# Kernel tuning notes

Measured on AMD Instinct MI355X. Metric: run time of the kernel, lower is better.

## Reference

```python
import jax, jax.numpy as jnp
import numpy as np

B, C, H, W = 8, 512, 32, 32
HEADS, TOPK = 8, 4


def setup_inputs() -> dict:
    key = jax.random.key(0)
    k1, k2 = jax.random.split(key, 2)
    x = jax.random.normal(k1, (B, C, H, W), dtype=jnp.float32)
    W_qkv = jax.random.normal(k2, (C, 3 * C), dtype=jnp.float32) / np.sqrt(C).astype(np.float32)
    b_qkv = jnp.zeros((3 * C,), dtype=jnp.float32)
    return {"x": x, "W_qkv": W_qkv, "b_qkv": b_qkv}


def reference(x, W_qkv, b_qkv):
    B_, C_, H_, W_ = x.shape
    h = HEADS
    d = C_ // h
    N = H_ * W_
    # (B, C, H, W) -> (B, N, C)
    xt = x.reshape(B_, C_, N).transpose(0, 2, 1)
    qkv = (xt @ W_qkv + b_qkv).reshape(B_, N, 3, h, d).transpose(2, 0, 3, 1, 4)
    q, k, v = qkv[0], qkv[1], qkv[2]            # each (B, h, N, d)
    attn = jnp.einsum('bhid,bhjd->bhij', q, k)  # dense (B, h, N, N) scores
    topk_w, topk_i = jax.lax.top_k(attn, TOPK)  # (B, h, N, K), sorted desc like torch.topk
    # gather v along token axis per (b, h): v_sel[b,h,i,t] = v[b,h,topk_i[b,h,i,t]]
    gather_bh = jax.vmap(jax.vmap(lambda vv, ii: vv[ii]))
    v_sel = gather_bh(v, topk_i)                # (B, h, N, K, d)
    w = jax.nn.softmax(topk_w, axis=-1)
    weighted_v = jnp.einsum('bhik,bhikd->bhid', w, v_sel)  # (B, h, N, d)
    out = (weighted_v * q).sum(axis=2)          # (B, h, d): original sums over tokens
    # original: out.transpose(1,2).reshape(B,C,H,W) -- only valid when H*W==1;
    # we return the same data flattened to (B, C).
    return out.transpose(0, 2, 1).reshape(B_, C_)
```

## Files before the change

### kernel.cpp

```cpp
#include <hip/hip_runtime.h>

#define NEG_INF (-3.402823466e+38f)

constexpr int Bc = 8, Cc = 512, Hc = 8, Dc = 64, Nc = 1024;
constexpr size_t QSZ = (size_t)Bc * Hc * Nc * Dc;
constexpr size_t XTSZ = (size_t)8192 * 512;
constexpr size_t WTSZ = (size_t)1536 * 512;

typedef __attribute__((ext_vector_type(8))) short short8;
typedef __attribute__((ext_vector_type(4))) float f32x4;
typedef unsigned short ushort_t;
typedef unsigned int uint_t;

__device__ __forceinline__ ushort_t f2bf(float x) {
  uint_t u = __float_as_uint(x);
  u += 0x7FFFu + ((u >> 16) & 1u);
  return (ushort_t)(u >> 16);
}
__device__ __forceinline__ float bf2f(ushort_t h) {
  return __uint_as_float(((uint_t)h) << 16);
}

__global__ __launch_bounds__(256) void conv_x(const float* __restrict__ x,
                                              ushort_t* __restrict__ xh,
                                              float* __restrict__ out) {
  __shared__ float t[64][65];
  const int b = blockIdx.z, c0 = blockIdx.y * 64, n0 = blockIdx.x * 64;
  const int tid = threadIdx.x;
  const int lc = tid & 63, lr = tid >> 6;
  int fb = (blockIdx.z * 8 + blockIdx.y) * 16 + blockIdx.x;
  if (fb < 16) out[fb * 256 + tid] = 0.f;
#pragma unroll
  for (int i = 0; i < 16; ++i) {
    int cc = lr + i * 4;
    t[cc][lc] = x[((size_t)(b * 512 + c0 + cc)) * 1024 + n0 + lc];
  }
  __syncthreads();
#pragma unroll
  for (int i = 0; i < 16; ++i) {
    int nn = lr + i * 4;
    xh[((size_t)(b * 1024 + n0 + nn)) * 512 + c0 + lc] = f2bf(t[lc][nn]);
  }
}

__global__ __launch_bounds__(256) void conv_w(const float* __restrict__ wq,
                                              ushort_t* __restrict__ wh,
                                              ushort_t* __restrict__ wl) {
  __shared__ float t[64][65];
  const int c0 = blockIdx.y * 64, j0 = blockIdx.x * 64;
  const int tid = threadIdx.x;
  const int lj = tid & 63, lr = tid >> 6;
#pragma unroll
  for (int i = 0; i < 16; ++i) {
    int cc = lr + i * 4;
    t[cc][lj] = wq[(size_t)(c0 + cc) * 1536 + j0 + lj];
  }
  __syncthreads();
#pragma unroll
  for (int i = 0; i < 16; ++i) {
    int jj = lr + i * 4;
    float v = t[lj][jj];
    ushort_t h = f2bf(v);
    size_t o = (size_t)(j0 + jj) * 512 + c0 + lj;
    wh[o] = h;
    wl[o] = f2bf(v - bf2f(h));
  }
}

__device__ __forceinline__ void stage_tile(ushort_t* lds, const ushort_t* g,
                                           int tid) {
  typedef const __attribute__((address_space(1))) unsigned int GU;
  typedef __attribute__((address_space(3))) unsigned int LU;
  {
    int l = tid, r = l >> 2, c = (l & 3) * 8;
    __builtin_amdgcn_global_load_lds((GU*)(g + (size_t)r * 512 + c),
                                     (LU*)(lds + (size_t)l * 8), 16, 0, 0);
  }
  {
    int l = tid + 256, r = l >> 2, c = (l & 3) * 8;
    __builtin_amdgcn_global_load_lds((GU*)(g + (size_t)r * 512 + c),
                                     (LU*)(lds + (size_t)l * 8), 16, 0, 0);
  }
}

__global__ __launch_bounds__(256) void qkv_gemm_mfma(
    const ushort_t* __restrict__ xth, const ushort_t* __restrict__ wth,
    const ushort_t* __restrict__ wtl, const float* __restrict__ bias,
    float* __restrict__ vbuf, float* __restrict__ kf, float* __restrict__ qf,
    ushort_t* __restrict__ khi, ushort_t* __restrict__ qhi) {
  __shared__ __align__(16) ushort_t Ah[128 * 32];
  __shared__ __align__(16) ushort_t Bh[128 * 32];
  __shared__ __align__(16) ushort_t Bl[128 * 32];

  const int m0 = blockIdx.x * 128, j0 = blockIdx.y * 128;
  const int tid = threadIdx.x;
  const int w = tid >> 6, l = tid & 63;
  const int lr = l & 15, lg = l >> 4;
  const int wr = w >> 1, wc = w & 1;

  f32x4 acc[4][4];
#pragma unroll
  for (int i = 0; i < 4; ++i)
#pragma unroll
    for (int j = 0; j < 4; ++j) acc[i][j] = (f32x4){0.f, 0.f, 0.f, 0.f};

  const ushort_t* xa = xth + (size_t)m0 * 512;
  const ushort_t* wa = wth + (size_t)j0 * 512;
  const ushort_t* wb = wtl + (size_t)j0 * 512;

  for (int s = 0; s < 16; ++s) {
    const int k0 = s * 32;
    stage_tile(Ah, xa + k0, tid);
    stage_tile(Bh, wa + k0, tid);
    stage_tile(Bl, wb + k0, tid);
    __syncthreads();

    short8 ah[4], bh[4], bl[4];
#pragma unroll
    for (int mi = 0; mi < 4; ++mi)
      ah[mi] = *(const short8*)&Ah[(wr * 64 + mi * 16 + lr) * 32 + lg * 8];
#pragma unroll
    for (int ji = 0; ji < 4; ++ji) {
      int ro = (wc * 64 + ji * 16 + lr) * 32 + lg * 8;
      bh[ji] = *(const short8*)&Bh[ro];
      bl[ji] = *(const short8*)&Bl[ro];
    }
#pragma unroll
    for (int mi = 0; mi < 4; ++mi)
#pragma unroll
      for (int ji = 0; ji < 4; ++ji) {
        acc[mi][ji] = __builtin_amdgcn_mfma_f32_16x16x32_bf16(
            ah[mi], bh[ji], acc[mi][ji], 0, 0, 0);
        acc[mi][ji] = __builtin_amdgcn_mfma_f32_16x16x32_bf16(
            ah[mi], bl[ji], acc[mi][ji], 0, 0, 0);
      }
    __syncthreads();
  }

  const int which = j0 >> 9;
  const int hh = ((j0 >> 6) + wc) & 7;
  float bias_r[4];
#pragma unroll
  for (int ji = 0; ji < 4; ++ji) bias_r[ji] = bias[j0 + wc * 64 + ji * 16 + lr];

#pragma unroll
  for (int mi = 0; mi < 4; ++mi)
#pragma unroll
    for (int t = 0; t < 4; ++t) {
      int m = m0 + wr * 64 + mi * 16 + lg * 4 + t;
      int b = m >> 10, n = m & 1023;
      size_t rb = ((size_t)(b * 8 + hh) << 16) + (size_t)n * 64;
#pragma unroll
      for (int ji = 0; ji < 4; ++ji) {
        float val = acc[mi][ji][t] + bias_r[ji];
        int dd = ji * 16 + lr;
        if (which == 2) {
          vbuf[rb + dd] = val;
        } else if (which == 0) {
          qhi[rb + dd] = f2bf(val);
          qf[rb + dd] = val;
        } else {
          khi[rb + dd] = f2bf(val);
          kf[rb + dd] = val;
        }
      }
    }
}

__device__ __forceinline__ float packkey(float s, uint_t j) {
  return __uint_as_float((__float_as_uint(s) & 0xFFFFFC00u) | j);
}

__device__ __forceinline__ void sort4f(float& a, float& b, float& c,
                                       float& d) {
  float t;
  t = fmaxf(a, b); b = fminf(a, b); a = t;
  t = fmaxf(c, d); d = fminf(c, d); c = t;
  t = fmaxf(a, c); c = fminf(a, c); a = t;
  t = fmaxf(b, d); d = fminf(b, d); b = t;
  t = fmaxf(b, c); c = fminf(b, c); b = t;
}

__device__ __forceinline__ void merge44f(float& s0, float& s1, float& s2,
                                         float& s3, float a, float b, float c,
                                         float d) {
  s0 = fmaxf(s0, d); s1 = fmaxf(s1, c); s2 = fmaxf(s2, b); s3 = fmaxf(s3, a);
  float t;
  t = fmaxf(s0, s2); s2 = fminf(s0, s2); s0 = t;
  t = fmaxf(s1, s3); s3 = fminf(s1, s3); s1 = t;
  t = fmaxf(s0, s1); s1 = fminf(s0, s1); s0 = t;
  t = fmaxf(s2, s3); s3 = fminf(s2, s3); s2 = t;
}

__device__ __forceinline__ void insert4(float sc, int jv, float& s0, float& s1,
                                        float& s2, float& s3, int& i0, int& i1,
                                        int& i2, int& i3) {
  bool c = sc > s3;
  s3 = c ? sc : s3; i3 = c ? jv : i3;
  c = s3 > s2;
  { float t = c ? s2 : s3; s2 = c ? s3 : s2; s3 = t;
    int q = c ? i2 : i3; i2 = c ? i3 : i2; i3 = q; }
  c = s2 > s1;
  { float t = c ? s1 : s2; s1 = c ? s2 : s1; s2 = t;
    int q = c ? i1 : i2; i1 = c ? i2 : i1; i2 = q; }
  c = s1 > s0;
  { float t = c ? s0 : s1; s0 = c ? s1 : s0; s1 = t;
    int q = c ? i0 : i1; i0 = c ? i1 : i0; i1 = q; }
}

__device__ __forceinline__ void stage_k_chunk(ushort_t* kt,
                                              const ushort_t* gk, int chunk,
                                              int tid) {
  typedef const __attribute__((address_space(1))) unsigned int GU;
  typedef __attribute__((address_space(3))) unsigned int LU;
#pragma unroll
  for (int ri = 0; ri < 4; ++ri) {
    int p = ri * 512 + tid;
    int row = p >> 3;
    int colu = (p & 7) << 3;
    int srcu = (chunk * 256 + row) * 64 + (colu ^ ((row & 7) << 3));
    __builtin_amdgcn_global_load_lds((GU*)(gk + srcu),
                                     (LU*)(kt + (size_t)p * 8), 16, 0, 0);
  }
}

__global__ __launch_bounds__(512, 4) void attn_topk_mfma(
    const ushort_t* __restrict__ khi, const ushort_t* __restrict__ qhi,
    const float* __restrict__ kf, const float* __restrict__ qf,
    const float* __restrict__ vg, float* __restrict__ out) {
  __shared__ __align__(16) ushort_t KT[2][256 * 64];
  __shared__ uint_t kLp[128][8];
  __shared__ float scS[128][8];
  __shared__ float wgt[128][4];
  __shared__ int widx[128][4];

  const int bid = blockIdx.x;
  const int bh = bid & 63;
  const int rg = bid >> 6;
  const int tid = threadIdx.x;
  const int w = tid >> 6, l = tid & 63;
  const int lg = l >> 4, lr = l & 15;

  const int bhbase = bh << 16;
  const int rowbase = rg * 128 + w * 16;
  const ushort_t* gk = khi + bhbase;

  short8 qh[2];
#pragma unroll
  for (int c2 = 0; c2 < 2; ++c2)
    qh[c2] = *(const short8*)(qhi + bhbase + (rowbase + lr) * 64 + c2 * 32 +
                              lg * 8);

  float Ka[4], Kb[4];
#pragma unroll
  for (int t = 0; t < 4; ++t) { Ka[t] = NEG_INF; Kb[t] = NEG_INF; }

  stage_k_chunk(KT[0], gk, 0, tid);
  __syncthreads();

  for (int c = 0; c < 4; ++c) {
    if (c < 3) stage_k_chunk(KT[(c + 1) & 1], gk, c + 1, tid);
    const ushort_t* kt = KT[c & 1];
    const uint_t jb0 = (uint_t)(c * 256) + (uint_t)(lg * 4);
    const int sw = lr & 7;
#pragma unroll
    for (int jtl = 0; jtl < 16; ++jtl) {
      const int rbase = (jtl * 16 + lr) * 64;
      short8 k0 = *(const short8*)&kt[rbase + ((lg ^ sw) << 3)];
      short8 k1 = *(const short8*)&kt[rbase + (((lg + 4) ^ sw) << 3)];
      f32x4 aA = {0.f, 0.f, 0.f, 0.f};
      aA = __builtin_amdgcn_mfma_f32_16x16x32_bf16(k0, qh[0], aA, 0, 0, 0);
      aA = __builtin_amdgcn_mfma_f32_16x16x32_bf16(k1, qh[1], aA, 0, 0, 0);
      const uint_t jbase = jb0 + (uint_t)(jtl * 16);
      float ca = packkey(aA[0], jbase);
      float cb = packkey(aA[1], jbase + 1);
      float cc = packkey(aA[2], jbase + 2);
      float cd = packkey(aA[3], jbase + 3);
      sort4f(ca, cb, cc, cd);
      if ((jtl & 1) == 0)
        merge44f(Ka[0], Ka[1], Ka[2], Ka[3], ca, cb, cc, cd);
      else
        merge44f(Kb[0], Kb[1], Kb[2], Kb[3], ca, cb, cc, cd);
    }
    __syncthreads();
  }

#pragma unroll
  for (int mask = 16; mask <= 32; mask <<= 1) {
    float a0 = __shfl_xor(Ka[0], mask), a1 = __shfl_xor(Ka[1], mask);
    float a2 = __shfl_xor(Ka[2], mask), a3 = __shfl_xor(Ka[3], mask);
    merge44f(Ka[0], Ka[1], Ka[2], Ka[3], a0, a1, a2, a3);
    float b0 = __shfl_xor(Kb[0], mask), b1 = __shfl_xor(Kb[1], mask);
    float b2 = __shfl_xor(Kb[2], mask), b3 = __shfl_xor(Kb[3], mask);
    merge44f(Kb[0], Kb[1], Kb[2], Kb[3], b0, b1, b2, b3);
  }
  if (l < 16) {
    int r = w * 16 + l;
#pragma unroll
    for (int t = 0; t < 4; ++t) {
      kLp[r][t] = __float_as_uint(Ka[t]);
      kLp[r][4 + t] = __float_as_uint(Kb[t]);
    }
  }

  {
    const int cand = l >> 3, dg = l & 7;
#pragma unroll 4
    for (int rr = 0; rr < 16; ++rr) {
      int r = w * 16 + rr;
      int j = (int)(kLp[r][cand] & 1023u);
      int qa = bhbase + (rg * 128 + r) * 64 + dg * 8;
      int ka = bhbase + j * 64 + dg * 8;
      f32x4 q0 = *(const f32x4*)(qf + qa);
      f32x4 q1 = *(const f32x4*)(qf + qa + 4);
      f32x4 k0 = *(const f32x4*)(kf + ka);
      f32x4 k1 = *(const f32x4*)(kf + ka + 4);
      float s = q0[0] * k0[0];
      s = fmaf(q0[1], k0[1], s);
      s = fmaf(q0[2], k0[2], s);
      s = fmaf(q0[3], k0[3], s);
      s = fmaf(q1[0], k1[0], s);
      s = fmaf(q1[1], k1[1], s);
      s = fmaf(q1[2], k1[2], s);
      s = fmaf(q1[3], k1[3], s);
      s += __shfl_xor(s, 1);
      s += __shfl_xor(s, 2);
      s += __shfl_xor(s, 4);
      if (dg == 0) scS[r][cand] = s;
    }
  }

  if (l < 16) {
    int r = w * 16 + l;
    float s0 = NEG_INF, s1 = NEG_INF, s2 = NEG_INF, s3 = NEG_INF;
    int i0 = 0, i1 = 0, i2 = 0, i3 = 0;
#pragma unroll
    for (int c8 = 0; c8 < 8; ++c8)
      insert4(scS[r][c8], (int)(kLp[r][c8] & 1023u), s0, s1, s2, s3, i0, i1,
              i2, i3);
    float m = s0;
    float e0 = expf(s0 - m), e1 = expf(s1 - m);
    float e2 = expf(s2 - m), e3 = expf(s3 - m);
    float inv = 1.f / (e0 + e1 + e2 + e3);
    wgt[r][0] = e0 * inv; wgt[r][1] = e1 * inv;
    wgt[r][2] = e2 * inv; wgt[r][3] = e3 * inv;
    widx[r][0] = i0; widx[r][1] = i1; widx[r][2] = i2; widx[r][3] = i3;
  }

  const float* vbh = vg + (size_t)bhbase;
  float acc = 0.f;
#pragma unroll 4
  for (int rr = 0; rr < 16; ++rr) {
    int r = w * 16 + rr;
    float w0 = wgt[r][0], w1 = wgt[r][1], w2 = wgt[r][2], w3 = wgt[r][3];
    int x0 = widx[r][0], x1 = widx[r][1], x2 = widx[r][2], x3 = widx[r][3];
    float wv = w0 * vbh[(size_t)x0 * 64 + l];
    wv = fmaf(w1, vbh[(size_t)x1 * 64 + l], wv);
    wv = fmaf(w2, vbh[(size_t)x2 * 64 + l], wv);
    wv = fmaf(w3, vbh[(size_t)x3 * 64 + l], wv);
    acc = fmaf(wv, qf[bhbase + (rg * 128 + r) * 64 + l], acc);
  }
  atomicAdd(&out[(bh >> 3) * Cc + l * Hc + (bh & 7)], acc);
}

extern "C" void kernel_launch(void* const* d_in, const int* in_sizes, int n_in,
                              void* d_out, int out_size, void* d_ws,
                              size_t ws_size, hipStream_t stream) {
  (void)in_sizes; (void)n_in; (void)out_size; (void)ws_size;
  const float* x = (const float*)d_in[0];
  const float* wq = (const float*)d_in[1];
  const float* bias = (const float*)d_in[2];
  float* out = (float*)d_out;

  float* vbuf = (float*)d_ws;
  float* kf = vbuf + QSZ;
  float* qf = kf + QSZ;
  ushort_t* khi = (ushort_t*)(qf + QSZ);
  ushort_t* qhi = khi + QSZ;
  ushort_t* xth = qhi + QSZ;
  ushort_t* wth = xth + XTSZ;
  ushort_t* wtl = wth + WTSZ;

  conv_x<<<dim3(16, 8, 8), 256, 0, stream>>>(x, xth, out);
  conv_w<<<dim3(24, 8), 256, 0, stream>>>(wq, wth, wtl);
  qkv_gemm_mfma<<<dim3(64, 12), 256, 0, stream>>>(xth, wth, wtl, bias, vbuf,
                                                  kf, qf, khi, qhi);
  attn_topk_mfma<<<dim3(512), 512, 0, stream>>>(khi, qhi, kf, qf, vbuf, out);
}
```

Measured before the change: 92.53 us.

## Split attention blocks to 64 rows with wave pairs sharing key tiles

The top-k attention kernel now handles 64 query rows per block instead of 128, so the launch grows to 1024 blocks. Each pair of waves splits the key tiles of a 128-key chunk between its two waves, giving 16 candidates per row that are rescored in fp32 and merged. The K staging buffer is halved and the scratch arrays are aliased onto it, cutting LDS so launch bounds can request 8 blocks. It adds extra block-wide barriers and more K staging traffic per query row in exchange for higher occupancy and more blocks.

```diff
diff --git a/kernel.cpp b/kernel.cpp
--- a/kernel.cpp
+++ b/kernel.cpp
@@ -214,25 +214,25 @@
   typedef const __attribute__((address_space(1))) unsigned int GU;
   typedef __attribute__((address_space(3))) unsigned int LU;
 #pragma unroll
-  for (int ri = 0; ri < 4; ++ri) {
+  for (int ri = 0; ri < 2; ++ri) {
     int p = ri * 512 + tid;
     int row = p >> 3;
     int colu = (p & 7) << 3;
-    int srcu = (chunk * 256 + row) * 64 + (colu ^ ((row & 7) << 3));
+    int srcu = (chunk * 128 + row) * 64 + (colu ^ ((row & 7) << 3));
     __builtin_amdgcn_global_load_lds((GU*)(gk + srcu),
                                      (LU*)(kt + (size_t)p * 8), 16, 0, 0);
   }
 }
 
-__global__ __launch_bounds__(512, 4) void attn_topk_mfma(
+__global__ __launch_bounds__(512, 8) void attn_topk_mfma(
     const ushort_t* __restrict__ khi, const ushort_t* __restrict__ qhi,
     const float* __restrict__ kf, const float* __restrict__ qf,
     const float* __restrict__ vg, float* __restrict__ out) {
-  __shared__ __align__(16) ushort_t KT[2][256 * 64];
-  __shared__ uint_t kLp[128][8];
-  __shared__ float scS[128][8];
-  __shared__ float wgt[128][4];
-  __shared__ int widx[128][4];
+  __shared__ __align__(16) ushort_t KT[2][128 * 64];
+  uint_t* kLp = (uint_t*)&KT[0][0];
+  float* scS = (float*)((char*)&KT[0][0] + 4096);
+  float* wgt = (float*)((char*)&KT[0][0] + 8192);
+  int* widx = (int*)((char*)&KT[0][0] + 9216);
 
   const int bid = blockIdx.x;
   const int bh = bid & 63;
@@ -240,9 +240,10 @@
   const int tid = threadIdx.x;
   const int w = tid >> 6, l = tid & 63;
   const int lg = l >> 4, lr = l & 15;
+  const int jp = w & 1, rs = w >> 1;
 
   const int bhbase = bh << 16;
-  const int rowbase = rg * 128 + w * 16;
+  const int rowbase = rg * 64 + rs * 16;
   const ushort_t* gk = khi + bhbase;
 
   short8 qh[2];
@@ -258,29 +259,29 @@
   stage_k_chunk(KT[0], gk, 0, tid);
   __syncthreads();
 
-  for (int c = 0; c < 4; ++c) {
-    if (c < 3) stage_k_chunk(KT[(c + 1) & 1], gk, c + 1, tid);
+  for (int c = 0; c < 8; ++c) {
+    if (c < 7) stage_k_chunk(KT[(c + 1) & 1], gk, c + 1, tid);
     const ushort_t* kt = KT[c & 1];
-    const uint_t jb0 = (uint_t)(c * 256) + (uint_t)(lg * 4);
-    const int sw = lr & 7;
-#pragma unroll
-    for (int jtl = 0; jtl < 16; ++jtl) {
+    const int sw = (lr & 7) << 3;
+#pragma unroll
+    for (int ji = 0; ji < 4; ++ji) {
+      const int jtl = jp + ji * 2;
       const int rbase = (jtl * 16 + lr) * 64;
-      short8 k0 = *(const short8*)&kt[rbase + ((lg ^ sw) << 3)];
-      short8 k1 = *(const short8*)&kt[rbase + (((lg + 4) ^ sw) << 3)];
+      short8 k0 = *(const short8*)&kt[rbase + ((lg << 3) ^ sw)];
+      short8 k1 = *(const short8*)&kt[rbase + (((lg + 4) << 3) ^ sw)];
       f32x4 aA = {0.f, 0.f, 0.f, 0.f};
       aA = __builtin_amdgcn_mfma_f32_16x16x32_bf16(k0, qh[0], aA, 0, 0, 0);
       aA = __builtin_amdgcn_mfma_f32_16x16x32_bf16(k1, qh[1], aA, 0, 0, 0);
-      const uint_t jbase = jb0 + (uint_t)(jtl * 16);
+      const uint_t jbase = (uint_t)(c * 128 + jtl * 16 + lg * 4);
       float ca = packkey(aA[0], jbase);
       float cb = packkey(aA[1], jbase + 1);
       float cc = packkey(aA[2], jbase + 2);
       float cd = packkey(aA[3], jbase + 3);
       sort4f(ca, cb, cc, cd);
-      if ((jtl & 1) == 0)
+      if (ji & 1)
+        merge44f(Kb[0], Kb[1], Kb[2], Kb[3], ca, cb, cc, cd);
+      else
         merge44f(Ka[0], Ka[1], Ka[2], Ka[3], ca, cb, cc, cd);
-      else
-        merge44f(Kb[0], Kb[1], Kb[2], Kb[3], ca, cb, cc, cd);
     }
     __syncthreads();
   }
@@ -295,21 +296,24 @@
     merge44f(Kb[0], Kb[1], Kb[2], Kb[3], b0, b1, b2, b3);
   }
   if (l < 16) {
-    int r = w * 16 + l;
+    int r = rs * 16 + l;
+    int s0 = jp * 8;
 #pragma unroll
     for (int t = 0; t < 4; ++t) {
-      kLp[r][t] = __float_as_uint(Ka[t]);
-      kLp[r][4 + t] = __float_as_uint(Kb[t]);
-    }
-  }
+      kLp[r * 16 + s0 + t] = __float_as_uint(Ka[t]);
+      kLp[r * 16 + s0 + 4 + t] = __float_as_uint(Kb[t]);
+    }
+  }
+  __syncthreads();
 
   {
     const int cand = l >> 3, dg = l & 7;
+    const int slot = jp * 8 + cand;
 #pragma unroll 4
     for (int rr = 0; rr < 16; ++rr) {
-      int r = w * 16 + rr;
-      int j = (int)(kLp[r][cand] & 1023u);
-      int qa = bhbase + (rg * 128 + r) * 64 + dg * 8;
+      int r = rs * 16 + rr;
+      int j = (int)(kLp[r * 16 + slot] & 1023u);
+      int qa = bhbase + (rg * 64 + r) * 64 + dg * 8;
       int ka = bhbase + j * 64 + dg * 8;
       f32x4 q0 = *(const f32x4*)(qf + qa);
       f32x4 q1 = *(const f32x4*)(qf + qa + 4);
@@ -326,39 +330,44 @@
       s += __shfl_xor(s, 1);
       s += __shfl_xor(s, 2);
       s += __shfl_xor(s, 4);
-      if (dg == 0) scS[r][cand] = s;
-    }
-  }
-
-  if (l < 16) {
-    int r = w * 16 + l;
+      if (dg == 0) scS[r * 16 + slot] = s;
+    }
+  }
+  __syncthreads();
+
+  if (jp == 0 && l < 16) {
+    int r = rs * 16 + l;
     float s0 = NEG_INF, s1 = NEG_INF, s2 = NEG_INF, s3 = NEG_INF;
     int i0 = 0, i1 = 0, i2 = 0, i3 = 0;
 #pragma unroll
-    for (int c8 = 0; c8 < 8; ++c8)
-      insert4(scS[r][c8], (int)(kLp[r][c8] & 1023u), s0, s1, s2, s3, i0, i1,
-              i2, i3);
+    for (int c16 = 0; c16 < 16; ++c16)
+      insert4(scS[r * 16 + c16], (int)(kLp[r * 16 + c16] & 1023u), s0, s1, s2,
+              s3, i0, i1, i2, i3);
     float m = s0;
     float e0 = expf(s0 - m), e1 = expf(s1 - m);
     float e2 = expf(s2 - m), e3 = expf(s3 - m);
     float inv = 1.f / (e0 + e1 + e2 + e3);
-    wgt[r][0] = e0 * inv; wgt[r][1] = e1 * inv;
-    wgt[r][2] = e2 * inv; wgt[r][3] = e3 * inv;
-    widx[r][0] = i0; widx[r][1] = i1; widx[r][2] = i2; widx[r][3] = i3;
-  }
+    wgt[r * 4 + 0] = e0 * inv; wgt[r * 4 + 1] = e1 * inv;
+    wgt[r * 4 + 2] = e2 * inv; wgt[r * 4 + 3] = e3 * inv;
+    widx[r * 4 + 0] = i0; widx[r * 4 + 1] = i1;
+    widx[r * 4 + 2] = i2; widx[r * 4 + 3] = i3;
+  }
+  __syncthreads();
 
   const float* vbh = vg + (size_t)bhbase;
   float acc = 0.f;
-#pragma unroll 4
-  for (int rr = 0; rr < 16; ++rr) {
-    int r = w * 16 + rr;
-    float w0 = wgt[r][0], w1 = wgt[r][1], w2 = wgt[r][2], w3 = wgt[r][3];
-    int x0 = widx[r][0], x1 = widx[r][1], x2 = widx[r][2], x3 = widx[r][3];
+#pragma unroll
+  for (int rr = 0; rr < 8; ++rr) {
+    int r = rs * 16 + jp * 8 + rr;
+    float w0 = wgt[r * 4 + 0], w1 = wgt[r * 4 + 1];
+    float w2 = wgt[r * 4 + 2], w3 = wgt[r * 4 + 3];
+    int x0 = widx[r * 4 + 0], x1 = widx[r * 4 + 1];
+    int x2 = widx[r * 4 + 2], x3 = widx[r * 4 + 3];
     float wv = w0 * vbh[(size_t)x0 * 64 + l];
     wv = fmaf(w1, vbh[(size_t)x1 * 64 + l], wv);
     wv = fmaf(w2, vbh[(size_t)x2 * 64 + l], wv);
     wv = fmaf(w3, vbh[(size_t)x3 * 64 + l], wv);
-    acc = fmaf(wv, qf[bhbase + (rg * 128 + r) * 64 + l], acc);
+    acc = fmaf(wv, qf[bhbase + (rg * 64 + r) * 64 + l], acc);
   }
   atomicAdd(&out[(bh >> 3) * Cc + l * Hc + (bh & 7)], acc);
 }
@@ -385,5 +394,5 @@
   conv_w<<<dim3(24, 8), 256, 0, stream>>>(wq, wth, wtl);
   qkv_gemm_mfma<<<dim3(64, 12), 256, 0, stream>>>(xth, wth, wtl, bias, vbuf,
                                                   kf, qf, khi, qhi);
-  attn_topk_mfma<<<dim3(512), 512, 0, stream>>>(khi, qhi, kf, qf, vbuf, out);
-}
+  attn_topk_mfma<<<dim3(1024), 512, 0, stream>>>(khi, qhi, kf, qf, vbuf, out);
+}
```

Result: slower. 101.9 us (+10.1%).
